# Kernel tuning notes

Measured on AMD Instinct MI355X. Metric: run time of the kernel, lower is better.

## Reference

```python
import jax, jax.numpy as jnp
import numpy as np

N_HEADS = 8
DIM = 128
BT, A, M = 2880, 10, 350  # bs*T, agents, map tokens (from forwards())
TOPK_SELF, TOPK_CROSS = 3, 32


def _split_heads(x, h):
    B, T, C = x.shape
    return x.reshape(B, T, h, C // h).transpose(0, 2, 1, 3)  # [B,h,T,hd]


def _biased_attn(q, k, v, pe, rel):
    """flex_attention with score_mod: score + pe[b,q,rel[b,q,kv],h], -inf where rel==-1.
    q:[B,H,Tq,d] k,v:[B,H,Tk,d] pe:[B,Tq,K,H] rel:[B,Tq,Tk] int"""
    d = q.shape[-1]
    scores = jnp.einsum('bhqd,bhkd->bhqk', q, k) / jnp.sqrt(jnp.asarray(d, q.dtype))
    safe = jnp.maximum(rel, 0)
    bias = jnp.take_along_axis(pe, safe[:, :, :, None], axis=2)  # [B,Tq,Tk,H]
    bias = bias.transpose(0, 3, 1, 2)                            # [B,H,Tq,Tk]
    scores = jnp.where(rel[:, None, :, :] > -1, scores + bias, -jnp.inf)
    attn = jax.nn.softmax(scores, axis=-1)
    out = jnp.einsum('bhqk,bhkd->bhqd', attn, v)
    B, H, Tq, hd = out.shape
    return out.transpose(0, 2, 1, 3).reshape(B, Tq, H * hd)


def _make_relation(key, B, Tq, Tk, topk):
    # topk random keys per query get offsets 0..topk-1 in ascending kv order; rest -1
    rand = jax.random.uniform(key, (B, Tq, Tk))
    idx = jnp.sort(jax.lax.top_k(rand, topk)[1], axis=-1)  # [B,Tq,topk]
    rel = jnp.full((B, Tq, Tk), -1, dtype=jnp.int32)
    b = jnp.arange(B)[:, None, None]
    qi = jnp.arange(Tq)[None, :, None]
    return rel.at[b, qi, idx].set(jnp.arange(topk, dtype=jnp.int32)[None, None, :])


def setup_inputs() -> dict:
    key = jax.random.key(0)
    ks = jax.random.split(key, 12)
    s = 0.02
    return {
        'a_token': jax.random.normal(ks[0], (BT, A, DIM), jnp.float32),
        'm_token': jax.random.normal(ks[1], (BT, M, DIM), jnp.float32),
        'a2m_pe': jax.random.uniform(ks[2], (BT, A, TOPK_CROSS, N_HEADS), jnp.float32),
        'a_pe': jax.random.uniform(ks[3], (BT, A, TOPK_SELF, N_HEADS), jnp.float32),
        'Wq': s * jax.random.normal(ks[4], (DIM, DIM), jnp.float32),
        'Wk': s * jax.random.normal(ks[5], (DIM, DIM), jnp.float32),
        'Wv': s * jax.random.normal(ks[6], (DIM, DIM), jnp.float32),
        'W_cross_proj': s * jax.random.normal(ks[7], (DIM, DIM), jnp.float32),
        'W_cattn': s * jax.random.normal(ks[8], (DIM, 3 * DIM), jnp.float32),
        'W_self_proj': s * jax.random.normal(ks[9], (DIM, DIM), jnp.float32),
        'a2m_relation': _make_relation(ks[10], BT, A, M, TOPK_CROSS),
        'a_relation': _make_relation(ks[11], BT, A, A, TOPK_SELF),
    }


def reference(a_token, m_token, a2m_pe, a_pe, Wq, Wk, Wv, W_cross_proj,
              W_cattn, W_self_proj, a2m_relation, a_relation):
    # cross attention: q from a_token, k/v from m_token (dropout=0 => identity)
    q = _split_heads(a_token @ Wq, N_HEADS)
    k = _split_heads(m_token @ Wk, N_HEADS)
    v = _split_heads(m_token @ Wv, N_HEADS)
    y = _biased_attn(q, k, v, a2m_pe, a2m_relation) @ W_cross_proj
    # self attention with fused qkv projection
    q2, k2, v2 = jnp.split(y @ W_cattn, 3, axis=-1)
    y2 = _biased_attn(_split_heads(q2, N_HEADS), _split_heads(k2, N_HEADS),
                      _split_heads(v2, N_HEADS), a_pe, a_relation)
    return y2 @ W_self_proj
```

## Files before the change

kernel.cpp:

```cpp
#include <hip/hip_runtime.h>
#include <hip/hip_bf16.h>


typedef __attribute__((ext_vector_type(4))) float f32x4;
typedef __attribute__((ext_vector_type(8))) short bf16x8v;
typedef __attribute__((ext_vector_type(4))) short short4v;

#define BT_N 2880
#define A_N  10
#define M_N  350
#define BQ_N (BT_N * A_N)
#define DIMC 128

static __device__ __forceinline__ short f2b(float x) {
    __hip_bfloat16 b = __float2bfloat16(x);
    return __builtin_bit_cast(short, b);
}
static __device__ __forceinline__ float b2f(short s) {
    unsigned u = ((unsigned)(unsigned short)s) << 16;
    return __builtin_bit_cast(float, u);
}

__global__ __launch_bounds__(256) void precompute_mats(
    const float* __restrict__ Wq, const float* __restrict__ Wk,
    const float* __restrict__ Wv, const float* __restrict__ Wcp,
    const float* __restrict__ Wc, const float* __restrict__ Wsp,
    short* __restrict__ S1t, short* __restrict__ VP1t,
    short* __restrict__ S2t, short* __restrict__ VP2z)
{
    int gid = blockIdx.x * 256 + threadIdx.x;
    int mat = gid >> 17;
    int idx = gid & 131071;
    float acc = 0.f;
    if (mat == 0) {
        int n = idx >> 7, c = idx & 127;
        int h = n >> 7, d = n & 127;
        #pragma unroll
        for (int t = 0; t < 16; ++t)
            acc += Wq[c * 128 + h * 16 + t] * Wk[d * 128 + h * 16 + t];
        S1t[idx] = f2b(acc * 0.25f);
    } else if (mat == 1) {
        int d = idx >> 10, o = idx & 1023;
        int h = o >> 7, c = o & 127;
        #pragma unroll
        for (int t = 0; t < 16; ++t)
            acc += Wv[c * 128 + h * 16 + t] * Wcp[(h * 16 + t) * 128 + d];
        VP1t[idx] = f2b(acc);
    } else if (mat == 2) {
        int n = idx >> 7, c = idx & 127;
        int h = n >> 7, d = n & 127;
        #pragma unroll
        for (int t = 0; t < 16; ++t)
            acc += Wc[c * 384 + h * 16 + t] * Wc[d * 384 + 128 + h * 16 + t];
        S2t[idx] = f2b(acc * 0.25f);
    } else {
        int n = idx >> 7, c = idx & 127;
        int h = n >> 7, d = n & 127;
        #pragma unroll
        for (int t = 0; t < 16; ++t)
            acc += Wc[c * 384 + 256 + h * 16 + t] * Wsp[(h * 16 + t) * 128 + d];
        VP2z[idx] = f2b(acc);
    }
}

__global__ __launch_bounds__(256) void conv_bf16(
    const float* __restrict__ in, short* __restrict__ out)
{
    int i = blockIdx.x * 256 + threadIdx.x;
    f32x4 a = ((const f32x4*)in)[2 * i];
    f32x4 b = ((const f32x4*)in)[2 * i + 1];
    bf16x8v t;
    t[0] = f2b(a.x); t[1] = f2b(a.y); t[2] = f2b(a.z); t[3] = f2b(a.w);
    t[4] = f2b(b.x); t[5] = f2b(b.y); t[6] = f2b(b.z); t[7] = f2b(b.w);
    ((bf16x8v*)out)[i] = t;
}

template<bool CF32>
__global__ __launch_bounds__(256) void gemm_bt(
    const short* __restrict__ Ap, const short* __restrict__ Bt,
    void* __restrict__ Cp, int M, int N, int K)
{
    __shared__ short As[128][72];
    __shared__ short Bs[128][72];
    const int tid  = threadIdx.x;
    const int bm   = blockIdx.y << 7, bn = blockIdx.x << 7;
    const int wave = tid >> 6, lane = tid & 63;
    const int wm   = (wave >> 1) << 6, wn = (wave & 1) << 6;
    const int row16 = lane & 15, kq = (lane >> 4) << 3;
    f32x4 acc[4][4] = {};

    for (int k0 = 0; k0 < K; k0 += 64) {
        #pragma unroll
        for (int i = 0; i < 4; ++i) {
            int g = (i << 8) + tid;
            int r = g >> 3, c = (g & 7) << 3;
            *(bf16x8v*)&As[r][c] = *(const bf16x8v*)(Ap + (size_t)(bm + r) * K + k0 + c);
        }
        #pragma unroll
        for (int i = 0; i < 4; ++i) {
            int g = (i << 8) + tid;
            int r = g >> 3, c = (g & 7) << 3;
            *(bf16x8v*)&Bs[r][c] = *(const bf16x8v*)(Bt + (size_t)(bn + r) * K + k0 + c);
        }
        __syncthreads();
        #pragma unroll
        for (int kk = 0; kk < 64; kk += 32) {
            bf16x8v afr[4], bfr[4];
            #pragma unroll
            for (int mi = 0; mi < 4; ++mi)
                afr[mi] = *(const bf16x8v*)&As[wm + (mi << 4) + row16][kq + kk];
            #pragma unroll
            for (int ni = 0; ni < 4; ++ni)
                bfr[ni] = *(const bf16x8v*)&Bs[wn + (ni << 4) + row16][kq + kk];
            #pragma unroll
            for (int mi = 0; mi < 4; ++mi)
                #pragma unroll
                for (int ni = 0; ni < 4; ++ni)
                    acc[mi][ni] = __builtin_amdgcn_mfma_f32_16x16x32_bf16(
                        afr[mi], bfr[ni], acc[mi][ni], 0, 0, 0);
        }
        __syncthreads();
    }

    const int col = lane & 15, rb = (lane >> 4) << 2;
    #pragma unroll
    for (int mi = 0; mi < 4; ++mi)
        #pragma unroll
        for (int ni = 0; ni < 4; ++ni)
            #pragma unroll
            for (int r = 0; r < 4; ++r) {
                int rr = bm + wm + (mi << 4) + rb + r;
                int cc = bn + wn + (ni << 4) + col;
                float v = acc[mi][ni][r];
                if (CF32) ((float*)Cp)[(size_t)rr * N + cc] = v;
                else      ((short*)Cp)[(size_t)rr * N + cc] = f2b(v);
            }
}

__global__ __launch_bounds__(256) void attn_cross(
    const float* __restrict__ m_token, const short* __restrict__ qS,
    const float* __restrict__ pe, const int* __restrict__ rel,
    short* __restrict__ u)
{
    __shared__ short mrows[32][136];
    __shared__ short qsr[16][136];
    __shared__ float sc[32][17];
    __shared__ float wts[8][33];
    __shared__ float peL[256];
    __shared__ int   selk[32];

    const int phys = blockIdx.x;
    const int b    = (phys & 7) * 360 + (phys >> 3) / A_N;
    const int q    = (phys >> 3) % A_N;
    const int bq   = b * A_N + q;
    const int tid  = threadIdx.x;
    const int wave = tid >> 6, lane = tid & 63;
    const int row16 = lane & 15, kq8 = (lane >> 4) << 3;

    const int* relrow = rel + (size_t)bq * M_N;
    for (int k = tid; k < M_N; k += 256) {
        int r = relrow[k];
        if (r >= 0) selk[r] = k;
    }
    if (tid < 128) {
        int h = tid >> 4, c8 = (tid & 15) << 3;
        *(bf16x8v*)&qsr[h][c8] = *(const bf16x8v*)(qS + (size_t)bq * 1024 + h * 128 + c8);
    }
    for (int g = tid; g < 1088; g += 256) ((short*)qsr)[1088 + g] = 0;
    peL[tid] = pe[(size_t)bq * 256 + tid];
    __syncthreads();

    {
        int r = tid >> 3, c16 = (tid & 7) << 4;
        const float* src = m_token + ((size_t)b * M_N + selk[r]) * DIMC + c16;
        f32x4 v0 = *(const f32x4*)(src);
        f32x4 v1 = *(const f32x4*)(src + 4);
        f32x4 v2 = *(const f32x4*)(src + 8);
        f32x4 v3 = *(const f32x4*)(src + 12);
        bf16x8v t0, t1;
        t0[0] = f2b(v0.x); t0[1] = f2b(v0.y); t0[2] = f2b(v0.z); t0[3] = f2b(v0.w);
        t0[4] = f2b(v1.x); t0[5] = f2b(v1.y); t0[6] = f2b(v1.z); t0[7] = f2b(v1.w);
        t1[0] = f2b(v2.x); t1[1] = f2b(v2.y); t1[2] = f2b(v2.z); t1[3] = f2b(v2.w);
        t1[4] = f2b(v3.x); t1[5] = f2b(v3.y); t1[6] = f2b(v3.z); t1[7] = f2b(v3.w);
        *(bf16x8v*)&mrows[r][c16]     = t0;
        *(bf16x8v*)&mrows[r][c16 + 8] = t1;
    }
    __syncthreads();

    if (wave < 2) {
        f32x4 acc = {0.f, 0.f, 0.f, 0.f};
        #pragma unroll
        for (int kc = 0; kc < 4; ++kc) {
            bf16x8v a  = *(const bf16x8v*)&mrows[(wave << 4) + row16][(kc << 5) + kq8];
            bf16x8v bb = *(const bf16x8v*)&qsr[row16][(kc << 5) + kq8];
            acc = __builtin_amdgcn_mfma_f32_16x16x32_bf16(a, bb, acc, 0, 0, 0);
        }
        const int rb4 = (lane >> 4) << 2;
        #pragma unroll
        for (int r = 0; r < 4; ++r)
            sc[(wave << 4) + rb4 + r][row16] = acc[r];
    }
    __syncthreads();

    {
        const int h = tid >> 5, r = tid & 31;
        float s = sc[r][h] + peL[r * 8 + h];
        float mx = s;
        #pragma unroll
        for (int off = 16; off; off >>= 1) mx = fmaxf(mx, __shfl_xor(mx, off, 32));
        float e = __expf(s - mx);
        float su = e;
        #pragma unroll
        for (int off = 16; off; off >>= 1) su += __shfl_xor(su, off, 32);
        wts[h][r] = e / su;
    }
    __syncthreads();

    {
        const int h = tid >> 5, d0 = (tid << 2) & 127;
        f32x4 acc = {0.f, 0.f, 0.f, 0.f};
        #pragma unroll
        for (int r = 0; r < 32; ++r) {
            float w = wts[h][r];
            short4v mv = *(const short4v*)&mrows[r][d0];
            acc.x += w * b2f(mv.x);
            acc.y += w * b2f(mv.y);
            acc.z += w * b2f(mv.z);
            acc.w += w * b2f(mv.w);
        }
        short4v t;
        t.x = f2b(acc.x); t.y = f2b(acc.y); t.z = f2b(acc.z); t.w = f2b(acc.w);
        *(short4v*)(u + (size_t)bq * 1024 + (tid << 2)) = t;
    }
}

__global__ __launch_bounds__(256) void tail_fused(
    const short* __restrict__ ybf, const short* __restrict__ S2t,
    const short* __restrict__ VP2z, const float* __restrict__ pe,
    const int* __restrict__ rel, float* __restrict__ outp)
{
    __shared__ short yL[48][136];
    __shared__ short TL[48][136];
    __shared__ short Bs[64][136];
    __shared__ float sw[4][10][3];
    __shared__ float peL[960];
    __shared__ int   selS[120];

    const int tid  = threadIdx.x;
    const int wave = tid >> 6, lane = tid & 63;
    const int row16 = lane & 15, kq8 = (lane >> 4) << 3, rb4 = (lane >> 4) << 2;
    const int B0row = blockIdx.x * 40;

    for (int g = tid; g < 640; g += 256) {
        int r = g >> 4, c8 = (g & 15) << 3;
        *(bf16x8v*)&yL[r][c8] = *(const bf16x8v*)(ybf + (size_t)(B0row + r) * 128 + c8);
    }
    for (int g = tid; g < 1088; g += 256) ((short*)yL)[40 * 136 + g] = 0;
    for (int g = tid; g < 400; g += 256) {
        int v = rel[(size_t)blockIdx.x * 400 + g];
        if (v >= 0) {
            int bb = g / 100, rem = g - bb * 100;
            int q = rem / 10, k = rem - q * 10;
            selS[bb * 30 + q * 3 + v] = k;
        }
    }
    for (int g = tid; g < 960; g += 256) peL[g] = pe[(size_t)blockIdx.x * 960 + g];
    __syncthreads();

    bf16x8v af[3][4];
    #pragma unroll
    for (int mt = 0; mt < 3; ++mt)
        #pragma unroll
        for (int kk = 0; kk < 4; ++kk)
            af[mt][kk] = *(const bf16x8v*)&yL[(mt << 4) + row16][(kk << 5) + kq8];

    f32x4 acc_out[5] = {};

    for (int h = 0; h < 8; ++h) {
        #pragma unroll
        for (int dh = 0; dh < 2; ++dh) {
            __syncthreads();
            #pragma unroll
            for (int i = 0; i < 4; ++i) {
                int g = (i << 8) + tid;
                int r = g >> 4, c8 = (g & 15) << 3;
                *(bf16x8v*)&Bs[r][c8] =
                    *(const bf16x8v*)(S2t + (size_t)(h * 128 + dh * 64 + r) * 128 + c8);
            }
            __syncthreads();
            bf16x8v bfr[4];
            #pragma unroll
            for (int kk = 0; kk < 4; ++kk)
                bfr[kk] = *(const bf16x8v*)&Bs[(wave << 4) + row16][(kk << 5) + kq8];
            f32x4 gacc[3] = {};
            #pragma unroll
            for (int mt = 0; mt < 3; ++mt)
                #pragma unroll
                for (int kk = 0; kk < 4; ++kk)
                    gacc[mt] = __builtin_amdgcn_mfma_f32_16x16x32_bf16(
                        af[mt][kk], bfr[kk], gacc[mt], 0, 0, 0);
            #pragma unroll
            for (int mt = 0; mt < 3; ++mt)
                #pragma unroll
                for (int r = 0; r < 4; ++r) {
                    int a = (mt << 4) + rb4 + r;
                    if (a < 40) TL[a][(dh << 6) + (wave << 4) + row16] = f2b(gacc[mt][r]);
                }
        }
        __syncthreads();

        if (tid < 120) {
            int bb = tid / 30, rem = tid - bb * 30, q = rem / 3, r = rem - q * 3;
            int k = selS[bb * 30 + q * 3 + r];
            const short* gq = &TL[bb * 10 + q][0];
            const short* yk = &yL[bb * 10 + k][0];
            float s = 0.f;
            #pragma unroll
            for (int d = 0; d < 128; d += 4) {
                short4v gv = *(const short4v*)(gq + d);
                short4v yv = *(const short4v*)(yk + d);
                s += b2f(gv.x) * b2f(yv.x) + b2f(gv.y) * b2f(yv.y)
                   + b2f(gv.z) * b2f(yv.z) + b2f(gv.w) * b2f(yv.w);
            }
            sw[bb][q][r] = s + peL[bb * 240 + q * 24 + r * 8 + h];
        }
        __syncthreads();
        if (tid < 40) {
            int bb = tid / 10, q = tid - bb * 10;
            float s0 = sw[bb][q][0], s1 = sw[bb][q][1], s2 = sw[bb][q][2];
            float mx = fmaxf(s0, fmaxf(s1, s2));
            float e0 = __expf(s0 - mx), e1 = __expf(s1 - mx), e2 = __expf(s2 - mx);
            float inv = 1.f / (e0 + e1 + e2);
            sw[bb][q][0] = e0 * inv; sw[bb][q][1] = e1 * inv; sw[bb][q][2] = e2 * inv;
        }

        #pragma unroll
        for (int dh = 0; dh < 2; ++dh) {
            __syncthreads();
            #pragma unroll
            for (int i = 0; i < 4; ++i) {
                int g = (i << 8) + tid;
                int r = g >> 4, c8 = (g & 15) << 3;
                *(bf16x8v*)&Bs[r][c8] =
                    *(const bf16x8v*)(VP2z + (size_t)(h * 128 + dh * 64 + r) * 128 + c8);
            }
            __syncthreads();
            bf16x8v bfr[4];
            #pragma unroll
            for (int kk = 0; kk < 4; ++kk)
                bfr[kk] = *(const bf16x8v*)&Bs[(wave << 4) + row16][(kk << 5) + kq8];
            f32x4 zacc[3] = {};
            #pragma unroll
            for (int mt = 0; mt < 3; ++mt)
                #pragma unroll
                for (int kk = 0; kk < 4; ++kk)
                    zacc[mt] = __builtin_amdgcn_mfma_f32_16x16x32_bf16(
                        af[mt][kk], bfr[kk], zacc[mt], 0, 0, 0);
            #pragma unroll
            for (int mt = 0; mt < 3; ++mt)
                #pragma unroll
                for (int r = 0; r < 4; ++r) {
                    int a = (mt << 4) + rb4 + r;
                    if (a < 40) TL[a][(dh << 6) + (wave << 4) + row16] = f2b(zacc[mt][r]);
                }
        }
        __syncthreads();

        #pragma unroll
        for (int i = 0; i < 5; ++i) {
            int g = (i << 8) + tid;
            int a = g >> 5, d4 = (g & 31) << 2;
            int bb = (a * 205) >> 11, q = a - bb * 10;
            int k0 = selS[bb * 30 + q * 3 + 0];
            int k1 = selS[bb * 30 + q * 3 + 1];
            int k2 = selS[bb * 30 + q * 3 + 2];
            float w0 = sw[bb][q][0], w1 = sw[bb][q][1], w2 = sw[bb][q][2];
            short4v z0 = *(const short4v*)&TL[bb * 10 + k0][d4];
            short4v z1 = *(const short4v*)&TL[bb * 10 + k1][d4];
            short4v z2 = *(const short4v*)&TL[bb * 10 + k2][d4];
            acc_out[i].x += w0 * b2f(z0.x) + w1 * b2f(z1.x) + w2 * b2f(z2.x);
            acc_out[i].y += w0 * b2f(z0.y) + w1 * b2f(z1.y) + w2 * b2f(z2.y);
            acc_out[i].z += w0 * b2f(z0.z) + w1 * b2f(z1.z) + w2 * b2f(z2.z);
            acc_out[i].w += w0 * b2f(z0.w) + w1 * b2f(z1.w) + w2 * b2f(z2.w);
        }
    }

    #pragma unroll
    for (int i = 0; i < 5; ++i) {
        int g = (i << 8) + tid;
        int a = g >> 5, d4 = (g & 31) << 2;
        *(f32x4*)(outp + (size_t)(B0row + a) * 128 + d4) = acc_out[i];
    }
}

extern "C" void kernel_launch(void* const* d_in, const int* in_sizes, int n_in,
                              void* d_out, int out_size, void* d_ws, size_t ws_size,
                              hipStream_t stream)
{
    const float* a_token = (const float*)d_in[0];
    const float* m_token = (const float*)d_in[1];
    const float* a2m_pe  = (const float*)d_in[2];
    const float* a_pe    = (const float*)d_in[3];
    const float* Wq      = (const float*)d_in[4];
    const float* Wk      = (const float*)d_in[5];
    const float* Wv      = (const float*)d_in[6];
    const float* Wcp     = (const float*)d_in[7];
    const float* Wc      = (const float*)d_in[8];
    const float* Wsp     = (const float*)d_in[9];
    const int*   a2m_rel = (const int*)d_in[10];
    const int*   a_rel   = (const int*)d_in[11];

    char* ws = (char*)d_ws;
    short* S1t  = (short*)(ws + 0);
    short* VP1t = (short*)(ws + 262144);
    short* S2t  = (short*)(ws + 524288);
    short* VP2z = (short*)(ws + 786432);
    short* buf1 = (short*)(ws + 1048576);
    short* buf2 = (short*)(ws + 1048576 + 58982400ull);
    short* ybf  = (short*)(ws + 1048576 + 2ull * 58982400ull);
    short* abf  = (short*)(ws + 126386176ull);
    float* outp = (float*)d_out;

    precompute_mats<<<dim3(2048), dim3(256), 0, stream>>>(
        Wq, Wk, Wv, Wcp, Wc, Wsp, S1t, VP1t, S2t, VP2z);

    conv_bf16<<<dim3(1800), dim3(256), 0, stream>>>(a_token, abf);

    gemm_bt<false><<<dim3(8, 225), dim3(256), 0, stream>>>(
        abf, S1t, (void*)buf1, BQ_N, 1024, 128);

    attn_cross<<<dim3(BQ_N), dim3(256), 0, stream>>>(
        m_token, buf1, a2m_pe, a2m_rel, buf2);

    gemm_bt<false><<<dim3(1, 225), dim3(256), 0, stream>>>(
        buf2, VP1t, (void*)ybf, BQ_N, 128, 1024);

    tail_fused<<<dim3(720), dim3(256), 0, stream>>>(
        ybf, S2t, VP2z, a_pe, a_rel, outp);
}
```

Baseline: 249.6 us.

## Fuse cross-attention output projection GEMM into tail kernel

The separate GEMM that turns the per-head attention output (1024 wide) into y (128 wide) is folded into the tail kernel. Each block now computes its 40 rows of y by looping over 16 K-chunks of the 1024 dimension with MFMA, staging u and VP1t tiles in shared memory that reuses the TL and B buffers. This drops one kernel launch and the round trip of y through global memory. In exchange each of the 720 blocks reloads the full VP1t matrix, and the low block count may leave this phase short on parallelism.

```diff
diff --git a/kernel.cpp b/kernel.cpp
--- a/kernel.cpp
+++ b/kernel.cpp
@@ -234,27 +234,69 @@
     }
 }
 
-__global__ __launch_bounds__(256) void tail_fused(
-    const short* __restrict__ ybf, const short* __restrict__ S2t,
-    const short* __restrict__ VP2z, const float* __restrict__ pe,
-    const int* __restrict__ rel, float* __restrict__ outp)
+__global__ __launch_bounds__(256) void tail_fused2(
+    const short* __restrict__ u_in, const short* __restrict__ VP1t,
+    const short* __restrict__ S2t, const short* __restrict__ VP2z,
+    const float* __restrict__ pe, const int* __restrict__ rel,
+    float* __restrict__ outp)
 {
     __shared__ short yL[48][136];
     __shared__ short TL[48][136];
-    __shared__ short Bs[64][136];
+    __shared__ char  BsRaw[18432];
     __shared__ float sw[4][10][3];
     __shared__ float peL[960];
     __shared__ int   selS[120];
+
+    short (*uL)[72]  = (short(*)[72])&TL[0][0];
+    short (*BsA)[136] = (short(*)[136])BsRaw;
+    short (*BsB)[72]  = (short(*)[72])BsRaw;
 
     const int tid  = threadIdx.x;
     const int wave = tid >> 6, lane = tid & 63;
     const int row16 = lane & 15, kq8 = (lane >> 4) << 3, rb4 = (lane >> 4) << 2;
     const int B0row = blockIdx.x * 40;
 
-    for (int g = tid; g < 640; g += 256) {
-        int r = g >> 4, c8 = (g & 15) << 3;
-        *(bf16x8v*)&yL[r][c8] = *(const bf16x8v*)(ybf + (size_t)(B0row + r) * 128 + c8);
-    }
+    f32x4 cy[3][2] = {};
+    for (int kc = 0; kc < 16; ++kc) {
+        __syncthreads();
+        for (int g = tid; g < 320; g += 256) {
+            int r = g >> 3, c8 = (g & 7) << 3;
+            *(bf16x8v*)&uL[r][c8] =
+                *(const bf16x8v*)(u_in + (size_t)(B0row + r) * 1024 + (kc << 6) + c8);
+        }
+        #pragma unroll
+        for (int i = 0; i < 4; ++i) {
+            int g = (i << 8) + tid;
+            int n = g >> 3, c8 = (g & 7) << 3;
+            *(bf16x8v*)&BsB[n][c8] =
+                *(const bf16x8v*)(VP1t + (size_t)n * 1024 + (kc << 6) + c8);
+        }
+        __syncthreads();
+        #pragma unroll
+        for (int ks = 0; ks < 2; ++ks) {
+            bf16x8v au[3];
+            #pragma unroll
+            for (int mt = 0; mt < 3; ++mt)
+                au[mt] = *(const bf16x8v*)&uL[(mt << 4) + row16][(ks << 5) + kq8];
+            #pragma unroll
+            for (int nt = 0; nt < 2; ++nt) {
+                bf16x8v bv = *(const bf16x8v*)&BsB[(wave << 5) + (nt << 4) + row16][(ks << 5) + kq8];
+                #pragma unroll
+                for (int mt = 0; mt < 3; ++mt)
+                    cy[mt][nt] = __builtin_amdgcn_mfma_f32_16x16x32_bf16(
+                        au[mt], bv, cy[mt][nt], 0, 0, 0);
+            }
+        }
+    }
+    #pragma unroll
+    for (int mt = 0; mt < 3; ++mt)
+        #pragma unroll
+        for (int nt = 0; nt < 2; ++nt)
+            #pragma unroll
+            for (int r = 0; r < 4; ++r) {
+                int a = (mt << 4) + rb4 + r;
+                if (a < 40) yL[a][(wave << 5) + (nt << 4) + row16] = f2b(cy[mt][nt][r]);
+            }
     for (int g = tid; g < 1088; g += 256) ((short*)yL)[40 * 136 + g] = 0;
     for (int g = tid; g < 400; g += 256) {
         int v = rel[(size_t)blockIdx.x * 400 + g];
@@ -284,14 +326,14 @@
             for (int i = 0; i < 4; ++i) {
                 int g = (i << 8) + tid;
                 int r = g >> 4, c8 = (g & 15) << 3;
-                *(bf16x8v*)&Bs[r][c8] =
+                *(bf16x8v*)&BsA[r][c8] =
                     *(const bf16x8v*)(S2t + (size_t)(h * 128 + dh * 64 + r) * 128 + c8);
             }
             __syncthreads();
             bf16x8v bfr[4];
             #pragma unroll
             for (int kk = 0; kk < 4; ++kk)
-                bfr[kk] = *(const bf16x8v*)&Bs[(wave << 4) + row16][(kk << 5) + kq8];
+                bfr[kk] = *(const bf16x8v*)&BsA[(wave << 4) + row16][(kk << 5) + kq8];
             f32x4 gacc[3] = {};
             #pragma unroll
             for (int mt = 0; mt < 3; ++mt)
@@ -341,14 +383,14 @@
             for (int i = 0; i < 4; ++i) {
                 int g = (i << 8) + tid;
                 int r = g >> 4, c8 = (g & 15) << 3;
-                *(bf16x8v*)&Bs[r][c8] =
+                *(bf16x8v*)&BsA[r][c8] =
                     *(const bf16x8v*)(VP2z + (size_t)(h * 128 + dh * 64 + r) * 128 + c8);
             }
             __syncthreads();
             bf16x8v bfr[4];
             #pragma unroll
             for (int kk = 0; kk < 4; ++kk)
-                bfr[kk] = *(const bf16x8v*)&Bs[(wave << 4) + row16][(kk << 5) + kq8];
+                bfr[kk] = *(const bf16x8v*)&BsA[(wave << 4) + row16][(kk << 5) + kq8];
             f32x4 zacc[3] = {};
             #pragma unroll
             for (int mt = 0; mt < 3; ++mt)
@@ -417,7 +459,6 @@
     short* VP2z = (short*)(ws + 786432);
     short* buf1 = (short*)(ws + 1048576);
     short* buf2 = (short*)(ws + 1048576 + 58982400ull);
-    short* ybf  = (short*)(ws + 1048576 + 2ull * 58982400ull);
     short* abf  = (short*)(ws + 126386176ull);
     float* outp = (float*)d_out;
 
@@ -432,9 +473,6 @@
     attn_cross<<<dim3(BQ_N), dim3(256), 0, stream>>>(
         m_token, buf1, a2m_pe, a2m_rel, buf2);
 
-    gemm_bt<false><<<dim3(1, 225), dim3(256), 0, stream>>>(
-        buf2, VP1t, (void*)ybf, BQ_N, 128, 1024);
-
-    tail_fused<<<dim3(720), dim3(256), 0, stream>>>(
-        ybf, S2t, VP2z, a_pe, a_rel, outp);
-}
+    tail_fused2<<<dim3(720), dim3(256), 0, stream>>>(
+        buf2, VP1t, S2t, VP2z, a_pe, a_rel, outp);
+}
```

After: 294.6 us. 1.18x slower.

## Replace folded Wq·Wk query projection with per-block K projection of gathered rows

Applied to the files above, without the earlier changes.

The cross-attention query path no longer precomputes an 8x-expanded query (a_token times the per-head folded Wq·Wk^T, 1024 wide). It computes a plain 128-wide q projection with a GEMM that reads fp32 a_token directly, which removes the separate bf16 conversion kernel. Each attention block then projects its 32 gathered m_token rows through Wk with MFMA and takes per-head dot products against q. This cuts the large intermediate write and read of 59 MB to about 7 MB, at the cost of extra per-block MFMA work and global reads of Wk.

```diff
diff --git a/kernel.cpp b/kernel.cpp
--- a/kernel.cpp
+++ b/kernel.cpp
@@ -25,20 +25,22 @@
     const float* __restrict__ Wq, const float* __restrict__ Wk,
     const float* __restrict__ Wv, const float* __restrict__ Wcp,
     const float* __restrict__ Wc, const float* __restrict__ Wsp,
-    short* __restrict__ S1t, short* __restrict__ VP1t,
-    short* __restrict__ S2t, short* __restrict__ VP2z)
+    short* __restrict__ Wqt, short* __restrict__ Wkt,
+    short* __restrict__ VP1t, short* __restrict__ S2t, short* __restrict__ VP2z)
 {
     int gid = blockIdx.x * 256 + threadIdx.x;
     int mat = gid >> 17;
     int idx = gid & 131071;
     float acc = 0.f;
     if (mat == 0) {
-        int n = idx >> 7, c = idx & 127;
-        int h = n >> 7, d = n & 127;
-        #pragma unroll
-        for (int t = 0; t < 16; ++t)
-            acc += Wq[c * 128 + h * 16 + t] * Wk[d * 128 + h * 16 + t];
-        S1t[idx] = f2b(acc * 0.25f);
+        if (idx < 16384) {
+            int n = idx >> 7, c = idx & 127;
+            Wqt[idx] = f2b(Wq[c * 128 + n] * 0.25f);
+        } else if (idx < 32768) {
+            int j = idx - 16384;
+            int n = j >> 7, c = j & 127;
+            Wkt[j] = f2b(Wk[c * 128 + n]);
+        }
     } else if (mat == 1) {
         int d = idx >> 10, o = idx & 1023;
         int h = o >> 7, c = o & 127;
@@ -63,21 +65,9 @@
     }
 }
 
-__global__ __launch_bounds__(256) void conv_bf16(
-    const float* __restrict__ in, short* __restrict__ out)
-{
-    int i = blockIdx.x * 256 + threadIdx.x;
-    f32x4 a = ((const f32x4*)in)[2 * i];
-    f32x4 b = ((const f32x4*)in)[2 * i + 1];
-    bf16x8v t;
-    t[0] = f2b(a.x); t[1] = f2b(a.y); t[2] = f2b(a.z); t[3] = f2b(a.w);
-    t[4] = f2b(b.x); t[5] = f2b(b.y); t[6] = f2b(b.z); t[7] = f2b(b.w);
-    ((bf16x8v*)out)[i] = t;
-}
-
-template<bool CF32>
+template<bool AF32, bool CF32>
 __global__ __launch_bounds__(256) void gemm_bt(
-    const short* __restrict__ Ap, const short* __restrict__ Bt,
+    const void* __restrict__ Ap, const short* __restrict__ Bt,
     void* __restrict__ Cp, int M, int N, int K)
 {
     __shared__ short As[128][72];
@@ -90,11 +80,25 @@
     f32x4 acc[4][4] = {};
 
     for (int k0 = 0; k0 < K; k0 += 64) {
-        #pragma unroll
-        for (int i = 0; i < 4; ++i) {
-            int g = (i << 8) + tid;
-            int r = g >> 3, c = (g & 7) << 3;
-            *(bf16x8v*)&As[r][c] = *(const bf16x8v*)(Ap + (size_t)(bm + r) * K + k0 + c);
+        if (AF32) {
+            const float* A = (const float*)Ap;
+            #pragma unroll
+            for (int i = 0; i < 8; ++i) {
+                int f = (i << 8) + tid;
+                int r = f >> 4, c = (f & 15) << 2;
+                f32x4 v = *(const f32x4*)(A + (size_t)(bm + r) * K + k0 + c);
+                short4v t;
+                t.x = f2b(v.x); t.y = f2b(v.y); t.z = f2b(v.z); t.w = f2b(v.w);
+                *(short4v*)&As[r][c] = t;
+            }
+        } else {
+            const short* A = (const short*)Ap;
+            #pragma unroll
+            for (int i = 0; i < 4; ++i) {
+                int g = (i << 8) + tid;
+                int r = g >> 3, c = (g & 7) << 3;
+                *(bf16x8v*)&As[r][c] = *(const bf16x8v*)(A + (size_t)(bm + r) * K + k0 + c);
+            }
         }
         #pragma unroll
         for (int i = 0; i < 4; ++i) {
@@ -137,14 +141,14 @@
             }
 }
 
-__global__ __launch_bounds__(256) void attn_cross(
-    const float* __restrict__ m_token, const short* __restrict__ qS,
-    const float* __restrict__ pe, const int* __restrict__ rel,
-    short* __restrict__ u)
+__global__ __launch_bounds__(256) void attn_cross2(
+    const float* __restrict__ m_token, const short* __restrict__ aq,
+    const short* __restrict__ Wkt, const float* __restrict__ pe,
+    const int* __restrict__ rel, short* __restrict__ u)
 {
     __shared__ short mrows[32][136];
-    __shared__ short qsr[16][136];
-    __shared__ float sc[32][17];
+    __shared__ float mkL[32][129];
+    __shared__ float aqf[128];
     __shared__ float wts[8][33];
     __shared__ float peL[256];
     __shared__ int   selk[32];
@@ -155,18 +159,14 @@
     const int bq   = b * A_N + q;
     const int tid  = threadIdx.x;
     const int wave = tid >> 6, lane = tid & 63;
-    const int row16 = lane & 15, kq8 = (lane >> 4) << 3;
+    const int row16 = lane & 15, kq8 = (lane >> 4) << 3, rb4 = (lane >> 4) << 2;
 
     const int* relrow = rel + (size_t)bq * M_N;
     for (int k = tid; k < M_N; k += 256) {
         int r = relrow[k];
         if (r >= 0) selk[r] = k;
     }
-    if (tid < 128) {
-        int h = tid >> 4, c8 = (tid & 15) << 3;
-        *(bf16x8v*)&qsr[h][c8] = *(const bf16x8v*)(qS + (size_t)bq * 1024 + h * 128 + c8);
-    }
-    for (int g = tid; g < 1088; g += 256) ((short*)qsr)[1088 + g] = 0;
+    if (tid < 128) aqf[tid] = b2f(aq[(size_t)bq * 128 + tid]);
     peL[tid] = pe[(size_t)bq * 256 + tid];
     __syncthreads();
 
@@ -187,24 +187,34 @@
     }
     __syncthreads();
 
-    if (wave < 2) {
-        f32x4 acc = {0.f, 0.f, 0.f, 0.f};
-        #pragma unroll
-        for (int kc = 0; kc < 4; ++kc) {
-            bf16x8v a  = *(const bf16x8v*)&mrows[(wave << 4) + row16][(kc << 5) + kq8];
-            bf16x8v bb = *(const bf16x8v*)&qsr[row16][(kc << 5) + kq8];
-            acc = __builtin_amdgcn_mfma_f32_16x16x32_bf16(a, bb, acc, 0, 0, 0);
-        }
-        const int rb4 = (lane >> 4) << 2;
-        #pragma unroll
-        for (int r = 0; r < 4; ++r)
-            sc[(wave << 4) + rb4 + r][row16] = acc[r];
+    {
+        const int mt = wave & 1, nh = wave >> 1;
+        #pragma unroll
+        for (int j = 0; j < 4; ++j) {
+            const int nt = (nh << 2) + j;
+            f32x4 acc = {0.f, 0.f, 0.f, 0.f};
+            #pragma unroll
+            for (int kc = 0; kc < 4; ++kc) {
+                bf16x8v a  = *(const bf16x8v*)&mrows[(mt << 4) + row16][(kc << 5) + kq8];
+                bf16x8v bb = *(const bf16x8v*)(Wkt +
+                    (size_t)(nt * 16 + row16) * 128 + (kc << 5) + kq8);
+                acc = __builtin_amdgcn_mfma_f32_16x16x32_bf16(a, bb, acc, 0, 0, 0);
+            }
+            #pragma unroll
+            for (int r = 0; r < 4; ++r)
+                mkL[(mt << 4) + rb4 + r][nt * 16 + row16] = acc[r];
+        }
     }
     __syncthreads();
 
     {
         const int h = tid >> 5, r = tid & 31;
-        float s = sc[r][h] + peL[r * 8 + h];
+        const float* mkr = &mkL[r][h << 4];
+        const float* aqh = &aqf[h << 4];
+        float s = 0.f;
+        #pragma unroll
+        for (int t = 0; t < 16; ++t) s += mkr[t] * aqh[t];
+        s += peL[r * 8 + h];
         float mx = s;
         #pragma unroll
         for (int off = 16; off; off >>= 1) mx = fmaxf(mx, __shfl_xor(mx, off, 32));
@@ -411,29 +421,27 @@
     const int*   a_rel   = (const int*)d_in[11];
 
     char* ws = (char*)d_ws;
-    short* S1t  = (short*)(ws + 0);
-    short* VP1t = (short*)(ws + 262144);
-    short* S2t  = (short*)(ws + 524288);
-    short* VP2z = (short*)(ws + 786432);
-    short* buf1 = (short*)(ws + 1048576);
-    short* buf2 = (short*)(ws + 1048576 + 58982400ull);
-    short* ybf  = (short*)(ws + 1048576 + 2ull * 58982400ull);
-    short* abf  = (short*)(ws + 126386176ull);
+    short* Wqt  = (short*)(ws + 0);
+    short* Wkt  = (short*)(ws + 32768);
+    short* VP1t = (short*)(ws + 65536);
+    short* S2t  = (short*)(ws + 327680);
+    short* VP2z = (short*)(ws + 589824);
+    short* aq   = (short*)(ws + 1048576);
+    short* buf2 = (short*)(ws + 1048576 + 7372800ull);
+    short* ybf  = (short*)(ws + 1048576 + 7372800ull + 58982400ull);
     float* outp = (float*)d_out;
 
     precompute_mats<<<dim3(2048), dim3(256), 0, stream>>>(
-        Wq, Wk, Wv, Wcp, Wc, Wsp, S1t, VP1t, S2t, VP2z);
-
-    conv_bf16<<<dim3(1800), dim3(256), 0, stream>>>(a_token, abf);
-
-    gemm_bt<false><<<dim3(8, 225), dim3(256), 0, stream>>>(
-        abf, S1t, (void*)buf1, BQ_N, 1024, 128);
-
-    attn_cross<<<dim3(BQ_N), dim3(256), 0, stream>>>(
-        m_token, buf1, a2m_pe, a2m_rel, buf2);
-
-    gemm_bt<false><<<dim3(1, 225), dim3(256), 0, stream>>>(
-        buf2, VP1t, (void*)ybf, BQ_N, 128, 1024);
+        Wq, Wk, Wv, Wcp, Wc, Wsp, Wqt, Wkt, VP1t, S2t, VP2z);
+
+    gemm_bt<true, false><<<dim3(1, 225), dim3(256), 0, stream>>>(
+        (const void*)a_token, Wqt, (void*)aq, BQ_N, 128, 128);
+
+    attn_cross2<<<dim3(BQ_N), dim3(256), 0, stream>>>(
+        m_token, aq, Wkt, a2m_pe, a2m_rel, buf2);
+
+    gemm_bt<false, false><<<dim3(1, 225), dim3(256), 0, stream>>>(
+        (const void*)buf2, VP1t, (void*)ybf, BQ_N, 128, 1024);
 
     tail_fused<<<dim3(720), dim3(256), 0, stream>>>(
         ybf, S2t, VP2z, a_pe, a_rel, outp);
```

Measured after the change: 416.2 us. 1.67x slower.
